# Performance work log

Hardware: AMD Instinct MI355X
Metric: run time of the kernel (lower is better)

Reference implementation:

```python
import jax, jax.numpy as jnp
import numpy as np

EPS = 1e-8          # torch CosineSimilarity eps
TEMPERATURE = 0.5
N = 4096            # device_size (== batch_size, world_size=1)
D = 256             # projection embedding dim


def setup_inputs() -> dict:
    key = jax.random.key(0)
    k1, k2 = jax.random.split(key)
    return {
        "z_i": jax.random.normal(k1, (N, D), dtype=jnp.float32),
        "z_j": jax.random.normal(k2, (N, D), dtype=jnp.float32),
    }


def reference(z_i, z_j):
    n = z_i.shape[0]
    # z_large = [z_i ; z_j]  (world_size == 1 layout)
    z = jnp.concatenate([z_i, z_j], axis=0)                      # [2N, D]
    zn = z / jnp.maximum(jnp.linalg.norm(z, axis=1, keepdims=True), EPS)
    zi_n, zj_n = zn[:n], zn[n:]
    # cosine similarity via normalize + GEMM (same math as CosineSimilarity(dim=2))
    sim_i = (zi_n @ zn.T) / TEMPERATURE                          # [N, 2N]
    sim_j = (zj_n @ zn.T) / TEMPERATURE                          # [N, 2N]
    idx = jnp.arange(n)
    neg_inf = jnp.finfo(sim_i.dtype).min
    # positives: sim_i row i vs column N+i; sim_j row i vs column i
    pos_i = sim_i[idx, n + idx]                                  # [N]
    pos_j = sim_j[idx, idx]                                      # [N]
    # exclude self-similarity from the softmax denominator
    sim_i_m = sim_i.at[idx, idx].set(neg_inf)
    sim_j_m = sim_j.at[idx, n + idx].set(neg_inf)
    # CrossEntropyLoss(sum) with label 0 on [pos, negs] == sum(lse - pos)
    lse_i = jax.scipy.special.logsumexp(sim_i_m, axis=1)
    lse_j = jax.scipy.special.logsumexp(sim_j_m, axis=1)
    loss_i = jnp.sum(lse_i - pos_i) / n
    loss_j = jnp.sum(lse_j - pos_j) / n
    return loss_i, loss_j
```

## Files before the change

kernel.cpp:

```cpp
#include <hip/hip_runtime.h>

#define NN   4096
#define TWON 8192
#define DD   256
#define TINV 2.0f
#define SCALE 1.69864363f
#define CS   16

typedef __attribute__((ext_vector_type(8)))  short v8s;
typedef __attribute__((ext_vector_type(16))) float v16f;

__device__ inline unsigned short f2bf(float f) {
  unsigned int u = __float_as_uint(f);
  u += 0x7FFFu + ((u >> 16) & 1u);
  return (unsigned short)(u >> 16);
}

__global__ void k_normpos(const float* __restrict__ zi, const float* __restrict__ zj,
                          unsigned short* __restrict__ zn, float* __restrict__ pospart) {
  int wid = threadIdx.x >> 6, lane = threadIdx.x & 63;
  int pr  = blockIdx.x * 2 + (wid >> 1);
  int isj = wid & 1;
  const float* src = (isj ? zj : zi) + (size_t)pr * DD;
  float4 v = *(const float4*)(src + lane * 4);
  float ss = v.x*v.x + v.y*v.y + v.z*v.z + v.w*v.w;
  #pragma unroll
  for (int m = 1; m < 64; m <<= 1) ss += __shfl_xor(ss, m, 64);
  float nrm = fmaxf(sqrtf(ss), 1e-8f);

  __shared__ float zbuf[2][DD];
  __shared__ float nbuf[2];
  if (!isj) {
    *(float4*)&zbuf[wid >> 1][lane * 4] = v;
    if (lane == 0) nbuf[wid >> 1] = nrm;
  }

  float sc = SCALE / nrm;
  ushort4 o;
  o.x = f2bf(v.x * sc); o.y = f2bf(v.y * sc);
  o.z = f2bf(v.z * sc); o.w = f2bf(v.w * sc);
  int zrow = (isj ? NN : 0) + pr;
  *(ushort4*)(zn + (size_t)zrow * DD + lane * 4) = o;

  __syncthreads();
  if (isj) {
    float4 a = *(const float4*)&zbuf[wid >> 1][lane * 4];
    float d = a.x*v.x + a.y*v.y + a.z*v.z + a.w*v.w;
    #pragma unroll
    for (int m = 1; m < 64; m <<= 1) d += __shfl_xor(d, m, 64);
    if (lane == 0) pospart[pr] = d * TINV / (nbuf[wid >> 1] * nrm);
  }
}

__global__ __launch_bounds__(256, 2) void k_main(const unsigned short* __restrict__ zn,
                                                 float* __restrict__ wsum) {
  const char* znb = (const char*)zn;
  int tid = threadIdx.x, wid = tid >> 6, lane = tid & 63;
  int rb = blockIdx.x >> 4, cs = blockIdx.x & 15;
  int wrow0 = rb * 256 + wid * 64;
  int lr = lane & 31, lg = lane >> 5;
  int cbase = cs * 512;
  int lane_src = lr * 512 + lg * 16;

  v8s afrag[2][16];
  #pragma unroll
  for (int h = 0; h < 2; ++h) {
    #pragma unroll
    for (int kk = 0; kk < 16; ++kk) {
      size_t off = (size_t)(wrow0 + h * 32 + lr) * 512 + kk * 32 + lg * 16;
      afrag[h][kk] = *(const v8s*)(znb + off);
    }
  }

  __shared__ char tile0[16384];
  __shared__ char tile1[16384];
  v16f sumv0, sumv1;
  #pragma unroll
  for (int q = 0; q < 16; ++q) { sumv0[q] = 0.f; sumv1[q] = 0.f; }

#define STAGE(CT, BUF) { \
    size_t gb = (size_t)(cbase + (CT) * 32) * 512; \
    _Pragma("unroll") \
    for (int p = 0; p < 4; ++p) { \
      int t = wid * 4 + p; \
      const char* s = znb + gb + t * 32 + lane_src; \
      __builtin_amdgcn_global_load_lds((const __attribute__((address_space(1))) void*)s, \
          (__attribute__((address_space(3))) void*)&(BUF)[t * 1024], 16, 0, 0); \
    } }

#define COMPUTE(BUF, CT) { \
    int ctile = cbase + (CT) * 32; \
    v16f acc0, acc1; \
    _Pragma("unroll") \
    for (int q = 0; q < 16; ++q) { acc0[q] = 0.f; acc1[q] = 0.f; } \
    const char* bb = &(BUF)[lg * 512 + lr * 16]; \
    _Pragma("unroll") \
    for (int kk = 0; kk < 16; ++kk) { \
      v8s b = *(const v8s*)(bb + kk * 1024); \
      acc0 = __builtin_amdgcn_mfma_f32_32x32x16_bf16(afrag[0][kk], b, acc0, 0, 0, 0); \
      acc1 = __builtin_amdgcn_mfma_f32_32x32x16_bf16(afrag[1][kk], b, acc1, 0, 0, 0); \
    } \
    if (ctile == wrow0 || ctile == wrow0 + 32) { \
      bool h0 = (ctile == wrow0); \
      _Pragma("unroll") \
      for (int q = 0; q < 16; ++q) { \
        int ro = 4 * lg + (q & 3) + 8 * (q >> 2); \
        float e0 = __builtin_amdgcn_exp2f(acc0[q]); \
        float e1 = __builtin_amdgcn_exp2f(acc1[q]); \
        if (h0 && ro == lr) e0 = 0.f; \
        if (!h0 && ro == lr) e1 = 0.f; \
        sumv0[q] += e0; sumv1[q] += e1; \
      } \
    } else { \
      _Pragma("unroll") \
      for (int q = 0; q < 16; ++q) { \
        sumv0[q] += __builtin_amdgcn_exp2f(acc0[q]); \
        sumv1[q] += __builtin_amdgcn_exp2f(acc1[q]); \
      } \
    } }

  STAGE(0, tile0);
  __syncthreads();
  for (int c2 = 0; c2 < 8; ++c2) {
    int ctB = c2 * 2 + 1;
    STAGE(ctB, tile1);
    COMPUTE(tile0, c2 * 2);
    __syncthreads();
    if (ctB + 1 < 16) STAGE(ctB + 1, tile0);
    COMPUTE(tile1, ctB);
    __syncthreads();
  }
#undef STAGE
#undef COMPUTE

  #pragma unroll
  for (int q = 0; q < 16; ++q) {
    float v0 = sumv0[q], v1 = sumv1[q];
    #pragma unroll
    for (int m = 1; m < 32; m <<= 1) {
      v0 += __shfl_xor(v0, m, 64);
      v1 += __shfl_xor(v1, m, 64);
    }
    sumv0[q] = v0; sumv1[q] = v1;
  }
  if (lr < 16) {
    int qi = lr;
    float o0 = 0.f, o1 = 0.f;
    #pragma unroll
    for (int q = 0; q < 16; ++q) {
      o0 = (q == qi) ? sumv0[q] : o0;
      o1 = (q == qi) ? sumv1[q] : o1;
    }
    int ro = 4 * lg + (qi & 3) + 8 * (qi >> 2);
    wsum[(size_t)(wrow0 + ro) * CS + cs] = o0;
    wsum[(size_t)(wrow0 + 32 + ro) * CS + cs] = o1;
  }
}

__global__ void k_lse(const float* __restrict__ wsum, float* __restrict__ lsepart) {
  int tid = threadIdx.x;
  int row = blockIdx.x * 128 + tid;
  const float4* p = (const float4*)(wsum + (size_t)row * 16);
  float4 a = p[0], b = p[1], c = p[2], d = p[3];
  float s = (((a.x + a.y) + (a.z + a.w)) + ((b.x + b.y) + (b.z + b.w)))
          + (((c.x + c.y) + (c.z + c.w)) + ((d.x + d.y) + (d.z + d.w)));
  float lse = logf(s);
  #pragma unroll
  for (int m = 1; m < 64; m <<= 1) lse += __shfl_xor(lse, m, 64);
  __shared__ float sb[2];
  if ((tid & 63) == 0) sb[tid >> 6] = lse;
  __syncthreads();
  if (tid == 0) lsepart[blockIdx.x] = sb[0] + sb[1];
}

__global__ void k_final(const float* __restrict__ lsepart, const float* __restrict__ pospart,
                        float* __restrict__ out) {
  int tid = threadIdx.x, wid = tid >> 6, lane = tid & 63;
  float li = (tid < 32) ? lsepart[tid] : 0.f;
  float lj = (tid >= 32 && tid < 64) ? lsepart[tid] : 0.f;
  float pp = 0.f;
  #pragma unroll
  for (int k = 0; k < 16; ++k) pp += pospart[tid + 256 * k];
  #pragma unroll
  for (int m = 1; m < 64; m <<= 1) {
    li += __shfl_xor(li, m, 64);
    lj += __shfl_xor(lj, m, 64);
    pp += __shfl_xor(pp, m, 64);
  }
  __shared__ float sI[4], sJ[4], sP[4];
  if (lane == 0) { sI[wid] = li; sJ[wid] = lj; sP[wid] = pp; }
  __syncthreads();
  if (tid == 0) {
    float SI = (sI[0] + sI[1]) + (sI[2] + sI[3]);
    float SJ = (sJ[0] + sJ[1]) + (sJ[2] + sJ[3]);
    float SP = (sP[0] + sP[1]) + (sP[2] + sP[3]);
    out[0] = (SI - SP) * (1.0f / NN);
    out[1] = (SJ - SP) * (1.0f / NN);
  }
}

extern "C" void kernel_launch(void* const* d_in, const int* in_sizes, int n_in,
                              void* d_out, int out_size, void* d_ws, size_t ws_size,
                              hipStream_t stream) {
  const float* zi = (const float*)d_in[0];
  const float* zj = (const float*)d_in[1];
  float* out = (float*)d_out;
  char* ws = (char*)d_ws;
  unsigned short* zn = (unsigned short*)ws;
  float* pospart = (float*)(ws + 4194304);
  float* lsepart = (float*)(ws + 4210688);
  float* wsum    = (float*)(ws + 4210944);

  k_normpos<<<2048, 256, 0, stream>>>(zi, zj, zn, pospart);
  k_main<<<512, 256, 0, stream>>>(zn, wsum);
  k_lse<<<64, 128, 0, stream>>>(wsum, lsepart);
  k_final<<<1, 256, 0, stream>>>(lsepart, pospart, out);
}
```

Before: 53.91 us.

## Halve rows per wave in main GEMM kernel to double occupancy and grid

Each wave now computes one 32-row MFMA tile instead of two, so each block covers 128 rows and the grid doubles to 1024 blocks. Launch bounds rise to 4 blocks per CU. The A-fragment and accumulator register footprint is halved to allow more resident waves and better latency hiding. In exchange, each staged B tile in LDS feeds half as many MFMAs, so LDS and global traffic per flop doubles.

```diff
diff --git a/kernel.cpp b/kernel.cpp
--- a/kernel.cpp
+++ b/kernel.cpp
@@ -52,31 +52,29 @@
   }
 }
 
-__global__ __launch_bounds__(256, 2) void k_main(const unsigned short* __restrict__ zn,
+__global__ __launch_bounds__(256, 4) void k_main(const unsigned short* __restrict__ zn,
                                                  float* __restrict__ wsum) {
   const char* znb = (const char*)zn;
   int tid = threadIdx.x, wid = tid >> 6, lane = tid & 63;
   int rb = blockIdx.x >> 4, cs = blockIdx.x & 15;
-  int wrow0 = rb * 256 + wid * 64;
+  int wrow0 = rb * 128 + wid * 32;
   int lr = lane & 31, lg = lane >> 5;
   int cbase = cs * 512;
   int lane_src = lr * 512 + lg * 16;
 
-  v8s afrag[2][16];
-  #pragma unroll
-  for (int h = 0; h < 2; ++h) {
-    #pragma unroll
-    for (int kk = 0; kk < 16; ++kk) {
-      size_t off = (size_t)(wrow0 + h * 32 + lr) * 512 + kk * 32 + lg * 16;
-      afrag[h][kk] = *(const v8s*)(znb + off);
-    }
+  v8s afrag[16];
+  #pragma unroll
+  for (int kk = 0; kk < 16; ++kk) {
+    size_t off = (size_t)(wrow0 + lr) * 512 + kk * 32 + lg * 16;
+    afrag[kk] = *(const v8s*)(znb + off);
+    asm volatile("" : "+v"(afrag[kk]));
   }
 
   __shared__ char tile0[16384];
   __shared__ char tile1[16384];
-  v16f sumv0, sumv1;
-  #pragma unroll
-  for (int q = 0; q < 16; ++q) { sumv0[q] = 0.f; sumv1[q] = 0.f; }
+  v16f sumv;
+  #pragma unroll
+  for (int q = 0; q < 16; ++q) sumv[q] = 0.f;
 
 #define STAGE(CT, BUF) { \
     size_t gb = (size_t)(cbase + (CT) * 32) * 512; \
@@ -90,33 +88,26 @@
 
 #define COMPUTE(BUF, CT) { \
     int ctile = cbase + (CT) * 32; \
-    v16f acc0, acc1; \
+    v16f acc; \
     _Pragma("unroll") \
-    for (int q = 0; q < 16; ++q) { acc0[q] = 0.f; acc1[q] = 0.f; } \
+    for (int q = 0; q < 16; ++q) acc[q] = 0.f; \
     const char* bb = &(BUF)[lg * 512 + lr * 16]; \
     _Pragma("unroll") \
     for (int kk = 0; kk < 16; ++kk) { \
       v8s b = *(const v8s*)(bb + kk * 1024); \
-      acc0 = __builtin_amdgcn_mfma_f32_32x32x16_bf16(afrag[0][kk], b, acc0, 0, 0, 0); \
-      acc1 = __builtin_amdgcn_mfma_f32_32x32x16_bf16(afrag[1][kk], b, acc1, 0, 0, 0); \
+      acc = __builtin_amdgcn_mfma_f32_32x32x16_bf16(afrag[kk], b, acc, 0, 0, 0); \
     } \
-    if (ctile == wrow0 || ctile == wrow0 + 32) { \
-      bool h0 = (ctile == wrow0); \
+    if (ctile == wrow0) { \
       _Pragma("unroll") \
       for (int q = 0; q < 16; ++q) { \
         int ro = 4 * lg + (q & 3) + 8 * (q >> 2); \
-        float e0 = __builtin_amdgcn_exp2f(acc0[q]); \
-        float e1 = __builtin_amdgcn_exp2f(acc1[q]); \
-        if (h0 && ro == lr) e0 = 0.f; \
-        if (!h0 && ro == lr) e1 = 0.f; \
-        sumv0[q] += e0; sumv1[q] += e1; \
+        float e = __builtin_amdgcn_exp2f(acc[q]); \
+        if (ro == lr) e = 0.f; \
+        sumv[q] += e; \
       } \
     } else { \
       _Pragma("unroll") \
-      for (int q = 0; q < 16; ++q) { \
-        sumv0[q] += __builtin_amdgcn_exp2f(acc0[q]); \
-        sumv1[q] += __builtin_amdgcn_exp2f(acc1[q]); \
-      } \
+      for (int q = 0; q < 16; ++q) sumv[q] += __builtin_amdgcn_exp2f(acc[q]); \
     } }
 
   STAGE(0, tile0);
@@ -135,25 +126,18 @@
 
   #pragma unroll
   for (int q = 0; q < 16; ++q) {
-    float v0 = sumv0[q], v1 = sumv1[q];
+    float v0 = sumv[q];
     #pragma unroll
-    for (int m = 1; m < 32; m <<= 1) {
-      v0 += __shfl_xor(v0, m, 64);
-      v1 += __shfl_xor(v1, m, 64);
-    }
-    sumv0[q] = v0; sumv1[q] = v1;
+    for (int m = 1; m < 32; m <<= 1) v0 += __shfl_xor(v0, m, 64);
+    sumv[q] = v0;
   }
   if (lr < 16) {
     int qi = lr;
-    float o0 = 0.f, o1 = 0.f;
+    float o0 = 0.f;
     #pragma unroll
-    for (int q = 0; q < 16; ++q) {
-      o0 = (q == qi) ? sumv0[q] : o0;
-      o1 = (q == qi) ? sumv1[q] : o1;
-    }
+    for (int q = 0; q < 16; ++q) o0 = (q == qi) ? sumv[q] : o0;
     int ro = 4 * lg + (qi & 3) + 8 * (qi >> 2);
     wsum[(size_t)(wrow0 + ro) * CS + cs] = o0;
-    wsum[(size_t)(wrow0 + 32 + ro) * CS + cs] = o1;
   }
 }
 
@@ -212,7 +196,7 @@
   float* wsum    = (float*)(ws + 4210944);
 
   k_normpos<<<2048, 256, 0, stream>>>(zi, zj, zn, pospart);
-  k_main<<<512, 256, 0, stream>>>(zn, wsum);
+  k_main<<<1024, 256, 0, stream>>>(zn, wsum);
   k_lse<<<64, 128, 0, stream>>>(wsum, lsepart);
   k_final<<<1, 256, 0, stream>>>(lsepart, pospart, out);
 }
```

Result: slower. 66.98 us (+24.2%).

## Exploit Gram matrix symmetry: compute upper-triangle tiles and emit row and column sums

Applied to the files above, without the earlier changes.

The similarity matrix is symmetric, so the main kernel now computes only 128x128 tiles on a cyclic band covering half the matrix (plus the diagonal tiles). Each off-diagonal tile contributes exp-sums both to its rows and, through a shared-memory column reduction, to its columns. Partial sums go into 65 slots per row, which the lse kernel then adds up. This roughly halves the MFMA and exp work. In exchange it adds a memset, more partial-sum traffic, smaller 128-thread blocks, and a longer reduction in k_lse.

```diff
diff --git a/kernel.cpp b/kernel.cpp
--- a/kernel.cpp
+++ b/kernel.cpp
@@ -5,7 +5,7 @@
 #define DD   256
 #define TINV 2.0f
 #define SCALE 1.69864363f
-#define CS   16
+#define NSLOT 65
 
 typedef __attribute__((ext_vector_type(8)))  short v8s;
 typedef __attribute__((ext_vector_type(16))) float v16f;
@@ -52,15 +52,19 @@
   }
 }
 
-__global__ __launch_bounds__(256, 2) void k_main(const unsigned short* __restrict__ zn,
-                                                 float* __restrict__ wsum) {
+__global__ __launch_bounds__(128) __attribute__((amdgpu_waves_per_eu(2, 2)))
+void k_main(const unsigned short* __restrict__ zn, float* __restrict__ wsum) {
   const char* znb = (const char*)zn;
   int tid = threadIdx.x, wid = tid >> 6, lane = tid & 63;
-  int rb = blockIdx.x >> 4, cs = blockIdx.x & 15;
-  int wrow0 = rb * 256 + wid * 64;
+  int bid = blockIdx.x;
+  int rb, t;
+  if (bid < 2048) { t = bid >> 6; rb = bid & 63; }
+  else            { t = 32;       rb = bid - 2048; }
+  int cb = (rb + t) & 63;
+  int row0 = rb * 128, col0 = cb * 128;
+  int wrow0 = row0 + wid * 64;
   int lr = lane & 31, lg = lane >> 5;
-  int cbase = cs * 512;
-  int lane_src = lr * 512 + lg * 16;
+  bool isDiag = (t == 0);
 
   v8s afrag[2][16];
   #pragma unroll
@@ -74,22 +78,21 @@
 
   __shared__ char tile0[16384];
   __shared__ char tile1[16384];
+  __shared__ float csum[2][128];
   v16f sumv0, sumv1;
   #pragma unroll
   for (int q = 0; q < 16; ++q) { sumv0[q] = 0.f; sumv1[q] = 0.f; }
 
-#define STAGE(CT, BUF) { \
-    size_t gb = (size_t)(cbase + (CT) * 32) * 512; \
-    _Pragma("unroll") \
-    for (int p = 0; p < 4; ++p) { \
-      int t = wid * 4 + p; \
-      const char* s = znb + gb + t * 32 + lane_src; \
+#define STAGE(T, BUF) { \
+    size_t gb = (size_t)(col0 + (T) * 32) * 512 + (tid & 31) * 512 + (tid >> 5) * 16; \
+    _Pragma("unroll") \
+    for (int p = 0; p < 8; ++p) { \
+      const char* s = znb + gb + p * 64; \
       __builtin_amdgcn_global_load_lds((const __attribute__((address_space(1))) void*)s, \
-          (__attribute__((address_space(3))) void*)&(BUF)[t * 1024], 16, 0, 0); \
+          (__attribute__((address_space(3))) void*)&(BUF)[p * 2048 + wid * 1024], 16, 0, 0); \
     } }
 
-#define COMPUTE(BUF, CT) { \
-    int ctile = cbase + (CT) * 32; \
+#define COMPUTE(BUF, T) { \
     v16f acc0, acc1; \
     _Pragma("unroll") \
     for (int q = 0; q < 16; ++q) { acc0[q] = 0.f; acc1[q] = 0.f; } \
@@ -100,36 +103,31 @@
       acc0 = __builtin_amdgcn_mfma_f32_32x32x16_bf16(afrag[0][kk], b, acc0, 0, 0, 0); \
       acc1 = __builtin_amdgcn_mfma_f32_32x32x16_bf16(afrag[1][kk], b, acc1, 0, 0, 0); \
     } \
-    if (ctile == wrow0 || ctile == wrow0 + 32) { \
-      bool h0 = (ctile == wrow0); \
-      _Pragma("unroll") \
-      for (int q = 0; q < 16; ++q) { \
-        int ro = 4 * lg + (q & 3) + 8 * (q >> 2); \
-        float e0 = __builtin_amdgcn_exp2f(acc0[q]); \
-        float e1 = __builtin_amdgcn_exp2f(acc1[q]); \
-        if (h0 && ro == lr) e0 = 0.f; \
-        if (!h0 && ro == lr) e1 = 0.f; \
-        sumv0[q] += e0; sumv1[q] += e1; \
-      } \
-    } else { \
-      _Pragma("unroll") \
-      for (int q = 0; q < 16; ++q) { \
-        sumv0[q] += __builtin_amdgcn_exp2f(acc0[q]); \
-        sumv1[q] += __builtin_amdgcn_exp2f(acc1[q]); \
-      } \
+    float c0 = 0.f, c1 = 0.f; \
+    bool d0 = isDiag && ((T) == 2 * wid); \
+    bool d1 = isDiag && ((T) == 2 * wid + 1); \
+    _Pragma("unroll") \
+    for (int q = 0; q < 16; ++q) { \
+      int ro = 4 * lg + (q & 3) + 8 * (q >> 2); \
+      float e0 = __builtin_amdgcn_exp2f(acc0[q]); \
+      float e1 = __builtin_amdgcn_exp2f(acc1[q]); \
+      if (d0 && ro == lr) e0 = 0.f; \
+      if (d1 && ro == lr) e1 = 0.f; \
+      sumv0[q] += e0; sumv1[q] += e1; \
+      c0 += e0; c1 += e1; \
+    } \
+    if (!isDiag) { \
+      float v = c0 + c1; \
+      v += __shfl_xor(v, 32, 64); \
+      if (lg == 0) csum[wid][(T) * 32 + lr] = v; \
     } }
 
   STAGE(0, tile0);
   __syncthreads();
-  for (int c2 = 0; c2 < 8; ++c2) {
-    int ctB = c2 * 2 + 1;
-    STAGE(ctB, tile1);
-    COMPUTE(tile0, c2 * 2);
-    __syncthreads();
-    if (ctB + 1 < 16) STAGE(ctB + 1, tile0);
-    COMPUTE(tile1, ctB);
-    __syncthreads();
-  }
+  STAGE(1, tile1);  COMPUTE(tile0, 0);  __syncthreads();
+  STAGE(2, tile0);  COMPUTE(tile1, 1);  __syncthreads();
+  STAGE(3, tile1);  COMPUTE(tile0, 2);  __syncthreads();
+                    COMPUTE(tile1, 3);
 #undef STAGE
 #undef COMPUTE
 
@@ -152,32 +150,37 @@
       o1 = (q == qi) ? sumv1[q] : o1;
     }
     int ro = 4 * lg + (qi & 3) + 8 * (qi >> 2);
-    wsum[(size_t)(wrow0 + ro) * CS + cs] = o0;
-    wsum[(size_t)(wrow0 + 32 + ro) * CS + cs] = o1;
+    wsum[(size_t)t * TWON + wrow0 + ro]      = o0;
+    wsum[(size_t)t * TWON + wrow0 + 32 + ro] = o1;
+  }
+
+  if (!isDiag) {
+    __syncthreads();
+    float v = csum[0][tid] + csum[1][tid];
+    wsum[(size_t)(32 + t) * TWON + col0 + tid] = v;
   }
 }
 
 __global__ void k_lse(const float* __restrict__ wsum, float* __restrict__ lsepart) {
-  int tid = threadIdx.x;
-  int row = blockIdx.x * 128 + tid;
-  const float4* p = (const float4*)(wsum + (size_t)row * 16);
-  float4 a = p[0], b = p[1], c = p[2], d = p[3];
-  float s = (((a.x + a.y) + (a.z + a.w)) + ((b.x + b.y) + (b.z + b.w)))
-          + (((c.x + c.y) + (c.z + c.w)) + ((d.x + d.y) + (d.z + d.w)));
+  int tid = threadIdx.x, wid = tid >> 6, lane = tid & 63;
+  int row = blockIdx.x * 256 + tid;
+  float s = 0.f;
+  #pragma unroll
+  for (int k = 0; k < NSLOT; ++k) s += wsum[(size_t)k * TWON + row];
   float lse = logf(s);
   #pragma unroll
   for (int m = 1; m < 64; m <<= 1) lse += __shfl_xor(lse, m, 64);
-  __shared__ float sb[2];
-  if ((tid & 63) == 0) sb[tid >> 6] = lse;
-  __syncthreads();
-  if (tid == 0) lsepart[blockIdx.x] = sb[0] + sb[1];
+  __shared__ float sb[4];
+  if (lane == 0) sb[wid] = lse;
+  __syncthreads();
+  if (tid == 0) lsepart[blockIdx.x] = (sb[0] + sb[1]) + (sb[2] + sb[3]);
 }
 
 __global__ void k_final(const float* __restrict__ lsepart, const float* __restrict__ pospart,
                         float* __restrict__ out) {
   int tid = threadIdx.x, wid = tid >> 6, lane = tid & 63;
-  float li = (tid < 32) ? lsepart[tid] : 0.f;
-  float lj = (tid >= 32 && tid < 64) ? lsepart[tid] : 0.f;
+  float li = (tid < 16) ? lsepart[tid] : 0.f;
+  float lj = (tid >= 16 && tid < 32) ? lsepart[tid] : 0.f;
   float pp = 0.f;
   #pragma unroll
   for (int k = 0; k < 16; ++k) pp += pospart[tid + 256 * k];
@@ -211,8 +214,9 @@
   float* lsepart = (float*)(ws + 4210688);
   float* wsum    = (float*)(ws + 4210944);
 
+  hipMemsetAsync(wsum, 0, (size_t)NSLOT * TWON * 4, stream);
   k_normpos<<<2048, 256, 0, stream>>>(zi, zj, zn, pospart);
-  k_main<<<512, 256, 0, stream>>>(zn, wsum);
-  k_lse<<<64, 128, 0, stream>>>(wsum, lsepart);
+  k_main<<<2080, 128, 0, stream>>>(zn, wsum);
+  k_lse<<<32, 256, 0, stream>>>(wsum, lsepart);
   k_final<<<1, 256, 0, stream>>>(lsepart, pospart, out);
 }
```

New measurement: 81.98 us. 1.52x slower.

## Split column range across more blocks and use vmcnt-based single-barrier pipeline

Applied to the files above, without the earlier changes.

Doubles the column-split factor so each block covers 256 columns in 8 tiles, launching 1024 blocks instead of 512 to improve occupancy and load balance across CUs. The double-buffered loop is rewritten with explicit s_waitcnt vmcnt and raw s_barrier plus sched barriers so the next tile's loads can stay in flight while the current tile is computed. The cost is that A fragments are reloaded twice as often per row, and the partial-sum buffer and LSE reduction grow to 32 entries per row.

```diff
diff --git a/kernel.cpp b/kernel.cpp
--- a/kernel.cpp
+++ b/kernel.cpp
@@ -5,7 +5,7 @@
 #define DD   256
 #define TINV 2.0f
 #define SCALE 1.69864363f
-#define CS   16
+#define CS   32
 
 typedef __attribute__((ext_vector_type(8)))  short v8s;
 typedef __attribute__((ext_vector_type(16))) float v16f;
@@ -56,10 +56,10 @@
                                                  float* __restrict__ wsum) {
   const char* znb = (const char*)zn;
   int tid = threadIdx.x, wid = tid >> 6, lane = tid & 63;
-  int rb = blockIdx.x >> 4, cs = blockIdx.x & 15;
+  int rb = blockIdx.x >> 5, cs = blockIdx.x & 31;
   int wrow0 = rb * 256 + wid * 64;
   int lr = lane & 31, lg = lane >> 5;
-  int cbase = cs * 512;
+  int cbase = cs * 256;
   int lane_src = lr * 512 + lg * 16;
 
   v8s afrag[2][16];
@@ -82,10 +82,10 @@
     size_t gb = (size_t)(cbase + (CT) * 32) * 512; \
     _Pragma("unroll") \
     for (int p = 0; p < 4; ++p) { \
-      int t = wid * 4 + p; \
-      const char* s = znb + gb + t * 32 + lane_src; \
+      int ti = wid * 4 + p; \
+      const char* s = znb + gb + ti * 32 + lane_src; \
       __builtin_amdgcn_global_load_lds((const __attribute__((address_space(1))) void*)s, \
-          (__attribute__((address_space(3))) void*)&(BUF)[t * 1024], 16, 0, 0); \
+          (__attribute__((address_space(3))) void*)&(BUF)[ti * 1024], 16, 0, 0); \
     } }
 
 #define COMPUTE(BUF, CT) { \
@@ -120,15 +120,21 @@
     } }
 
   STAGE(0, tile0);
-  __syncthreads();
-  for (int c2 = 0; c2 < 8; ++c2) {
-    int ctB = c2 * 2 + 1;
-    STAGE(ctB, tile1);
-    COMPUTE(tile0, c2 * 2);
-    __syncthreads();
-    if (ctB + 1 < 16) STAGE(ctB + 1, tile0);
-    COMPUTE(tile1, ctB);
-    __syncthreads();
+  #pragma unroll 1
+  for (int t = 0; t < 8; ++t) {
+    char* cur = (t & 1) ? tile1 : tile0;
+    char* nxt = (t & 1) ? tile0 : tile1;
+    if (t < 7) {
+      STAGE(t + 1, nxt);
+      asm volatile("s_waitcnt vmcnt(4)" ::: "memory");
+    } else {
+      asm volatile("s_waitcnt vmcnt(0)" ::: "memory");
+    }
+    __builtin_amdgcn_sched_barrier(0);
+    __builtin_amdgcn_s_barrier();
+    __builtin_amdgcn_sched_barrier(0);
+    COMPUTE(cur, t);
+    __builtin_amdgcn_s_barrier();
   }
 #undef STAGE
 #undef COMPUTE
@@ -160,10 +166,13 @@
 __global__ void k_lse(const float* __restrict__ wsum, float* __restrict__ lsepart) {
   int tid = threadIdx.x;
   int row = blockIdx.x * 128 + tid;
-  const float4* p = (const float4*)(wsum + (size_t)row * 16);
-  float4 a = p[0], b = p[1], c = p[2], d = p[3];
-  float s = (((a.x + a.y) + (a.z + a.w)) + ((b.x + b.y) + (b.z + b.w)))
-          + (((c.x + c.y) + (c.z + c.w)) + ((d.x + d.y) + (d.z + d.w)));
+  const float4* p = (const float4*)(wsum + (size_t)row * CS);
+  float s = 0.f;
+  #pragma unroll
+  for (int q = 0; q < 8; ++q) {
+    float4 a = p[q];
+    s += (a.x + a.y) + (a.z + a.w);
+  }
   float lse = logf(s);
   #pragma unroll
   for (int m = 1; m < 64; m <<= 1) lse += __shfl_xor(lse, m, 64);
@@ -212,7 +221,7 @@
   float* wsum    = (float*)(ws + 4210944);
 
   k_normpos<<<2048, 256, 0, stream>>>(zi, zj, zn, pospart);
-  k_main<<<512, 256, 0, stream>>>(zn, wsum);
+  k_main<<<1024, 256, 0, stream>>>(zn, wsum);
   k_lse<<<64, 128, 0, stream>>>(wsum, lsepart);
   k_final<<<1, 256, 0, stream>>>(lsepart, pospart, out);
 }
```

After: 60.10 us. 11.5% more time.
